# Performance work log

Hardware: AMD Instinct MI355X
Metric: run time of the kernel (lower is better)

## Reference

```python
import jax, jax.numpy as jnp
import numpy as np

TOP_K = 2


def setup_inputs() -> dict:
    key = jax.random.key(0)
    k1, k2, k3, k4 = jax.random.split(key, 4)
    B, S, D, H, E = 2, 2048, 1024, 4096, 8
    x = jax.random.normal(k1, (B, S, D), dtype=jnp.float32)
    router_w = jax.random.normal(k2, (E, D), dtype=jnp.float32) * 0.01  # nn.Linear(d, E).weight
    # kaiming-ish scaling for FFN weights
    w1 = jax.random.normal(k3, (E, H, D), dtype=jnp.float32) * (2.0 / D) ** 0.5
    b1 = jnp.zeros((E, H), dtype=jnp.float32)
    w2 = jax.random.normal(k4, (E, D, H), dtype=jnp.float32) * (2.0 / H) ** 0.5
    b2 = jnp.zeros((E, D), dtype=jnp.float32)
    return {"x": x, "router_w": router_w, "w1": w1, "b1": b1, "w2": w2, "b2": b2}


def reference(x, router_w, w1, b1, w2, b2):
    B, S, D = x.shape
    E = w1.shape[0]
    T = B * S
    x_flat = x.reshape(T, D)

    # Router: logits -> softmax -> top-k -> renormalize (eval mode: no jitter)
    logits = jnp.einsum('td,ed->te', x_flat, router_w)
    probs = jax.nn.softmax(logits, axis=-1)
    topw, topi = jax.lax.top_k(probs, TOP_K)                 # [T, k]
    topw = topw / jnp.sum(topw, axis=-1, keepdims=True)

    # Per-token combine weight for each expert: cw[t, e] = sum_k topw[t,k] * (topi[t,k]==e)
    cw = jnp.zeros((T, E), dtype=x.dtype)
    cw = cw.at[jnp.arange(T)[:, None], topi].add(topw)       # [T, E]

    # Expert FFNs (exact-erf GELU like torch F.gelu); combine weighted outputs.
    out = jnp.zeros((T, w2.shape[1]), dtype=x.dtype)
    for e in range(E):
        h = jax.nn.gelu(x_flat @ w1[e].T + b1[e], approximate=False)
        o = h @ w2[e].T + b2[e]
        out = out + cw[:, e:e + 1] * o
    return out.reshape(B, S, -1)
```

## Files before the change

kernel.cpp:

```cpp
#include <hip/hip_runtime.h>
#include <stdint.h>

typedef __attribute__((ext_vector_type(8))) short short8;
typedef __attribute__((ext_vector_type(4))) float floatx4;

#define T_TOK 4096
#define D_DIM 1024
#define H_DIM 4096
#define E_NUM 8
#define MAX_TILES 71

static __device__ __forceinline__ ushort f2bf(float f) {
    uint32_t u = __float_as_uint(f);
    u += 0x7FFF + ((u >> 16) & 1);
    return (ushort)(u >> 16);
}

static __device__ __forceinline__ uint4 pack8(float4 a, float4 b) {
    union { ushort u[8]; uint4 v; } r;
    r.u[0] = f2bf(a.x); r.u[1] = f2bf(a.y); r.u[2] = f2bf(a.z); r.u[3] = f2bf(a.w);
    r.u[4] = f2bf(b.x); r.u[5] = f2bf(b.y); r.u[6] = f2bf(b.z); r.u[7] = f2bf(b.w);
    return r.v;
}

static __device__ __forceinline__ void gl_lds16(const void* g, void* l) {
    __builtin_amdgcn_global_load_lds(
        (const __attribute__((address_space(1))) uint32_t*)g,
        (__attribute__((address_space(3))) uint32_t*)l, 16, 0, 0);
}

__global__ __launch_bounds__(256) void cvt_all_kernel(
    const float* __restrict__ x,  ushort* __restrict__ xbf,
    const float* __restrict__ w1, ushort* __restrict__ w1bf,
    const float* __restrict__ w2, ushort* __restrict__ w2bf)
{
    const size_t NX = (size_t)T_TOK * D_DIM;
    const size_t NW = (size_t)E_NUM * H_DIM * D_DIM;
    size_t i = ((size_t)blockIdx.x * 256 + threadIdx.x) * 8;
    const float* src; ushort* dst; size_t j;
    if (i < NX)           { src = x;  dst = xbf;  j = i; }
    else if (i < NX + NW) { src = w1; dst = w1bf; j = i - NX; }
    else                  { src = w2; dst = w2bf; j = i - NX - NW; }
    float4 a = *(const float4*)(src + j);
    float4 b = *(const float4*)(src + j + 4);
    *(uint4*)(dst + j) = pack8(a, b);
}

__global__ __launch_bounds__(256) void router_kernel(
    const float* __restrict__ x, const float* __restrict__ rw,
    int* __restrict__ counts, int* __restrict__ topi, float* __restrict__ topw)
{
    __shared__ float rwS[E_NUM * D_DIM];
    int tid = threadIdx.x;
    for (int i = tid; i < E_NUM * D_DIM / 4; i += 256)
        ((float4*)rwS)[i] = ((const float4*)rw)[i];
    __syncthreads();

    int wave = tid >> 6, lane = tid & 63;
    int t = blockIdx.x * 4 + wave;
    const float* xr = x + (size_t)t * D_DIM;

    float acc[E_NUM];
#pragma unroll
    for (int e = 0; e < E_NUM; e++) acc[e] = 0.f;

    float xv[16];
#pragma unroll
    for (int j = 0; j < 4; j++)
        *(float4*)&xv[j * 4] = ((const float4*)xr)[lane * 4 + j];
#pragma unroll
    for (int j = 0; j < 16; j++) {
        int idx = lane * 16 + j;
#pragma unroll
        for (int e = 0; e < E_NUM; e++)
            acc[e] += xv[j] * rwS[e * D_DIM + idx];
    }
#pragma unroll
    for (int e = 0; e < E_NUM; e++)
        for (int off = 32; off > 0; off >>= 1)
            acc[e] += __shfl_xor(acc[e], off, 64);

    if (lane == 0) {
        float mx = acc[0];
        for (int e = 1; e < E_NUM; e++) mx = fmaxf(mx, acc[e]);
        float p[E_NUM];
        for (int e = 0; e < E_NUM; e++) p[e] = expf(acc[e] - mx);
        int i0 = 0;
        for (int e = 1; e < E_NUM; e++) if (p[e] > p[i0]) i0 = e;
        int i1 = (i0 == 0) ? 1 : 0;
        for (int e = 0; e < E_NUM; e++) if (e != i0 && p[e] > p[i1]) i1 = e;
        float w0 = p[i0], w1 = p[i1], sw = w0 + w1;
        w0 /= sw; w1 /= sw;
        topi[t * 2] = i0; topi[t * 2 + 1] = i1;
        topw[t * 2] = w0; topw[t * 2 + 1] = w1;
        atomicAdd(&counts[i0], 1);
        atomicAdd(&counts[i1], 1);
    }
}

__global__ void offsets_tiles_kernel(const int* __restrict__ counts,
                                     int* __restrict__ offsets, int* __restrict__ cursors,
                                     int* __restrict__ tile_e, int* __restrict__ tile_m0)
{
    if (threadIdx.x == 0 && blockIdx.x == 0) {
        int off = 0, n = 0;
        for (int e = 0; e < E_NUM; e++) {
            offsets[e] = off; cursors[e] = off; off += counts[e];
            for (int m0 = 0; m0 < counts[e]; m0 += 128) {
                tile_e[n] = e; tile_m0[n] = m0; n++;
            }
        }
        for (; n < MAX_TILES; n++) tile_e[n] = -1;
    }
}

__global__ __launch_bounds__(256) void assign_kernel(
    const int* __restrict__ topi, const float* __restrict__ topw,
    int* __restrict__ cursors, int* __restrict__ pair_token, float* __restrict__ pair_w,
    int* __restrict__ ppos)
{
    int t = blockIdx.x * 256 + threadIdx.x;
    if (t >= T_TOK) return;
    for (int k = 0; k < 2; k++) {
        int e = topi[t * 2 + k];
        int pos = atomicAdd(&cursors[e], 1);
        pair_token[pos] = t;
        pair_w[pos] = topw[t * 2 + k];
        ppos[t * 2 + k] = pos;
    }
}

__global__ __launch_bounds__(256) void ffn1_kernel(
    const ushort* __restrict__ xbf, const ushort* __restrict__ w1bf,
    const float* __restrict__ bias1,
    const int* __restrict__ counts, const int* __restrict__ offsets,
    const int* __restrict__ tile_e, const int* __restrict__ tile_m0,
    const int* __restrict__ pair_token, ushort* __restrict__ h)
{
    int e = tile_e[blockIdx.x];
    if (e < 0) return;
    int m0 = tile_m0[blockIdx.x];
    int cnt = counts[e];
    int off = offsets[e];
    int n0 = blockIdx.y * 128;

    __shared__ ushort As[128 * 32];
    __shared__ ushort Bs[128 * 32];

    const int t = threadIdx.x;
    const int wave = t >> 6, lane = t & 63;
    const int wm = (wave >> 1) * 64, wn = (wave & 1) * 64;
    const int quad = lane >> 4, l16 = lane & 15;

    const int r0 = t >> 2;
    const int jb = t & 3;
    const int s0 = (r0 >> 1) & 3;
    const int csrc = (jb ^ s0) * 8;

    int grA0 = m0 + r0;        if (grA0 >= cnt) grA0 = cnt - 1;
    int grA1 = m0 + r0 + 64;   if (grA1 >= cnt) grA1 = cnt - 1;
    const ushort* aS0 = xbf + (size_t)pair_token[off + grA0] * D_DIM + csrc;
    const ushort* aS1 = xbf + (size_t)pair_token[off + grA1] * D_DIM + csrc;
    const ushort* bS0 = w1bf + ((size_t)e * H_DIM + n0 + r0) * D_DIM + csrc;
    const ushort* bS1 = bS0 + (size_t)64 * D_DIM;

    char* AsB = (char*)As;
    char* BsB = (char*)Bs;
    const int ldsW = wave * 1024;

    const int swz = (((l16 >> 1) & 3) ^ quad) * 16;
    int aOff[4], bOff[4];
#pragma unroll
    for (int i = 0; i < 4; i++) {
        aOff[i] = (wm + i * 16 + l16) * 64 + swz;
        bOff[i] = (wn + i * 16 + l16) * 64 + swz;
    }

    floatx4 acc[4][4] = {};

    for (int k0 = 0; k0 < D_DIM; k0 += 32) {
        __syncthreads();
        gl_lds16(aS0 + k0, AsB + ldsW);
        gl_lds16(aS1 + k0, AsB + 4096 + ldsW);
        gl_lds16(bS0 + k0, BsB + ldsW);
        gl_lds16(bS1 + k0, BsB + 4096 + ldsW);
        __syncthreads();

        short8 av[4], bv[4];
#pragma unroll
        for (int i = 0; i < 4; i++) av[i] = *(const short8*)(AsB + aOff[i]);
#pragma unroll
        for (int i = 0; i < 4; i++) bv[i] = *(const short8*)(BsB + bOff[i]);
#pragma unroll
        for (int mi = 0; mi < 4; mi++)
#pragma unroll
            for (int ni = 0; ni < 4; ni++)
                acc[mi][ni] = __builtin_amdgcn_mfma_f32_16x16x32_bf16(av[mi], bv[ni], acc[mi][ni], 0, 0, 0);
    }

    float bb[4];
#pragma unroll
    for (int ni = 0; ni < 4; ni++) bb[ni] = bias1[e * H_DIM + n0 + wn + ni * 16 + l16];

#pragma unroll
    for (int mi = 0; mi < 4; mi++) {
#pragma unroll
        for (int reg = 0; reg < 4; reg++) {
            int gm = m0 + wm + mi * 16 + quad * 4 + reg;
            if (gm < cnt) {
                ushort* hrow = h + (size_t)(off + gm) * H_DIM + n0 + wn;
#pragma unroll
                for (int ni = 0; ni < 4; ni++) {
                    float v = acc[mi][ni][reg] + bb[ni];
                    v = 0.5f * v * (1.f + erff(v * 0.70710678118654752f));
                    hrow[ni * 16 + l16] = f2bf(v);
                }
            }
        }
    }
}

__global__ __launch_bounds__(256) void ffn2_kernel(
    const ushort* __restrict__ h, const ushort* __restrict__ w2bf,
    const float* __restrict__ bias2,
    const int* __restrict__ counts, const int* __restrict__ offsets,
    const int* __restrict__ tile_e, const int* __restrict__ tile_m0,
    const float* __restrict__ pair_w, float* __restrict__ o_pair)
{
    int e = tile_e[blockIdx.x];
    if (e < 0) return;
    int m0 = tile_m0[blockIdx.x];
    int cnt = counts[e];
    int off = offsets[e];
    int n0 = blockIdx.y * 128;

    __shared__ ushort As[128 * 32];
    __shared__ ushort Bs[128 * 32];

    const int t = threadIdx.x;
    const int wave = t >> 6, lane = t & 63;
    const int wm = (wave >> 1) * 64, wn = (wave & 1) * 64;
    const int quad = lane >> 4, l16 = lane & 15;

    const int r0 = t >> 2;
    const int jb = t & 3;
    const int s0 = (r0 >> 1) & 3;
    const int csrc = (jb ^ s0) * 8;

    int grA0 = m0 + r0;        if (grA0 >= cnt) grA0 = cnt - 1;
    int grA1 = m0 + r0 + 64;   if (grA1 >= cnt) grA1 = cnt - 1;
    const ushort* aS0 = h + (size_t)(off + grA0) * H_DIM + csrc;
    const ushort* aS1 = h + (size_t)(off + grA1) * H_DIM + csrc;
    const ushort* bS0 = w2bf + ((size_t)e * D_DIM + n0 + r0) * H_DIM + csrc;
    const ushort* bS1 = bS0 + (size_t)64 * H_DIM;

    char* AsB = (char*)As;
    char* BsB = (char*)Bs;
    const int ldsW = wave * 1024;

    const int swz = (((l16 >> 1) & 3) ^ quad) * 16;
    int aOff[4], bOff[4];
#pragma unroll
    for (int i = 0; i < 4; i++) {
        aOff[i] = (wm + i * 16 + l16) * 64 + swz;
        bOff[i] = (wn + i * 16 + l16) * 64 + swz;
    }

    floatx4 acc[4][4] = {};

    for (int k0 = 0; k0 < H_DIM; k0 += 32) {
        __syncthreads();
        gl_lds16(aS0 + k0, AsB + ldsW);
        gl_lds16(aS1 + k0, AsB + 4096 + ldsW);
        gl_lds16(bS0 + k0, BsB + ldsW);
        gl_lds16(bS1 + k0, BsB + 4096 + ldsW);
        __syncthreads();

        short8 av[4], bv[4];
#pragma unroll
        for (int i = 0; i < 4; i++) av[i] = *(const short8*)(AsB + aOff[i]);
#pragma unroll
        for (int i = 0; i < 4; i++) bv[i] = *(const short8*)(BsB + bOff[i]);
#pragma unroll
        for (int mi = 0; mi < 4; mi++)
#pragma unroll
            for (int ni = 0; ni < 4; ni++)
                acc[mi][ni] = __builtin_amdgcn_mfma_f32_16x16x32_bf16(av[mi], bv[ni], acc[mi][ni], 0, 0, 0);
    }

    float bb[4];
#pragma unroll
    for (int ni = 0; ni < 4; ni++) bb[ni] = bias2[e * D_DIM + n0 + wn + ni * 16 + l16];

#pragma unroll
    for (int mi = 0; mi < 4; mi++) {
#pragma unroll
        for (int reg = 0; reg < 4; reg++) {
            int gm = m0 + wm + mi * 16 + quad * 4 + reg;
            if (gm < cnt) {
                float wgt = pair_w[off + gm];
                float* orow = o_pair + (size_t)(off + gm) * D_DIM + n0 + wn;
#pragma unroll
                for (int ni = 0; ni < 4; ni++)
                    orow[ni * 16 + l16] = (acc[mi][ni][reg] + bb[ni]) * wgt;
            }
        }
    }
}

__global__ __launch_bounds__(256) void combine_kernel(
    const float* __restrict__ o_pair, const int* __restrict__ ppos,
    float* __restrict__ out)
{
    int t = blockIdx.x;
    int d = threadIdx.x * 4;
    size_t p0 = (size_t)ppos[t * 2] * D_DIM;
    size_t p1 = (size_t)ppos[t * 2 + 1] * D_DIM;
    float4 a = *(const float4*)(o_pair + p0 + d);
    float4 b = *(const float4*)(o_pair + p1 + d);
    float4 r;
    r.x = a.x + b.x; r.y = a.y + b.y; r.z = a.z + b.z; r.w = a.w + b.w;
    *(float4*)(out + (size_t)t * D_DIM + d) = r;
}

extern "C" void kernel_launch(void* const* d_in, const int* in_sizes, int n_in,
                              void* d_out, int out_size, void* d_ws, size_t ws_size,
                              hipStream_t stream)
{
    const float* x  = (const float*)d_in[0];
    const float* rw = (const float*)d_in[1];
    const float* w1 = (const float*)d_in[2];
    const float* b1 = (const float*)d_in[3];
    const float* w2 = (const float*)d_in[4];
    const float* b2 = (const float*)d_in[5];
    float* out = (float*)d_out;

    char* ws = (char*)d_ws;
    int*   counts     = (int*)(ws + 0);
    int*   cursors    = (int*)(ws + 256);
    int*   offsets    = (int*)(ws + 512);
    int*   tile_e     = (int*)(ws + 1024);
    int*   tile_m0    = (int*)(ws + 1536);
    int*   topi       = (int*)(ws + 2048);
    float* topw       = (float*)(ws + 34816);
    int*   pair_token = (int*)(ws + 67584);
    float* pair_w     = (float*)(ws + 100352);
    int*   ppos       = (int*)(ws + 133120);
    ushort* xbf  = (ushort*)(ws + 165888);
    ushort* w1bf = (ushort*)(ws + 8554496ULL);
    ushort* w2bf = (ushort*)(ws + 75663360ULL);
    ushort* h    = (ushort*)(ws + 142772224ULL);
    float* o_pair = (float*)(ws + 8554496ULL);

    hipMemsetAsync(counts, 0, 32, stream);

    const size_t NTOT = (size_t)T_TOK * D_DIM + 2ULL * E_NUM * H_DIM * D_DIM;
    cvt_all_kernel<<<NTOT / 2048, 256, 0, stream>>>(x, xbf, w1, w1bf, w2, w2bf);

    router_kernel<<<T_TOK / 4, 256, 0, stream>>>(x, rw, counts, topi, topw);
    offsets_tiles_kernel<<<1, 64, 0, stream>>>(counts, offsets, cursors, tile_e, tile_m0);
    assign_kernel<<<T_TOK / 256, 256, 0, stream>>>(topi, topw, cursors, pair_token, pair_w, ppos);

    dim3 g1(MAX_TILES, H_DIM / 128, 1);
    ffn1_kernel<<<g1, 256, 0, stream>>>(xbf, w1bf, b1, counts, offsets, tile_e, tile_m0, pair_token, h);

    dim3 g2(MAX_TILES, D_DIM / 128, 1);
    ffn2_kernel<<<g2, 256, 0, stream>>>(h, w2bf, b2, counts, offsets, tile_e, tile_m0, pair_w, o_pair);

    combine_kernel<<<T_TOK, 256, 0, stream>>>(o_pair, ppos, out);
}
```

Before: 814.9 us.

## Double K-tile depth to 64 and split FFN2 K dimension across two planes

Both expert GEMM kernels now stage a 64-wide K slice per iteration with an 8-way XOR swizzle, halving barrier pairs per unit of work. FFN2 additionally splits its K=4096 reduction into two halves over gridDim.z and writes partial results to two separate planes, which the combine kernel sums. This raises FFN2 parallelism (its grid was only 71x8 tiles) at the cost of an extra fp32 partial-output write and read and doubled LDS usage per block.

```diff
diff --git a/kernel.cpp b/kernel.cpp
--- a/kernel.cpp
+++ b/kernel.cpp
@@ -9,6 +9,7 @@
 #define H_DIM 4096
 #define E_NUM 8
 #define MAX_TILES 71
+#define PLANE (8192ULL * 1024ULL)
 
 static __device__ __forceinline__ ushort f2bf(float f) {
     uint32_t u = __float_as_uint(f);
@@ -144,58 +145,67 @@
     int off = offsets[e];
     int n0 = blockIdx.y * 128;
 
-    __shared__ ushort As[128 * 32];
-    __shared__ ushort Bs[128 * 32];
+    __shared__ ushort As[128 * 64];
+    __shared__ ushort Bs[128 * 64];
 
     const int t = threadIdx.x;
     const int wave = t >> 6, lane = t & 63;
     const int wm = (wave >> 1) * 64, wn = (wave & 1) * 64;
     const int quad = lane >> 4, l16 = lane & 15;
 
-    const int r0 = t >> 2;
-    const int jb = t & 3;
-    const int s0 = (r0 >> 1) & 3;
-    const int csrc = (jb ^ s0) * 8;
-
-    int grA0 = m0 + r0;        if (grA0 >= cnt) grA0 = cnt - 1;
-    int grA1 = m0 + r0 + 64;   if (grA1 >= cnt) grA1 = cnt - 1;
-    const ushort* aS0 = xbf + (size_t)pair_token[off + grA0] * D_DIM + csrc;
-    const ushort* aS1 = xbf + (size_t)pair_token[off + grA1] * D_DIM + csrc;
-    const ushort* bS0 = w1bf + ((size_t)e * H_DIM + n0 + r0) * D_DIM + csrc;
-    const ushort* bS1 = bS0 + (size_t)64 * D_DIM;
-
+    const int rsub = lane >> 3;
+    const int cpos = lane & 7;
+    const int srcElem = (cpos ^ rsub) * 8;
+
+    const ushort* aP[4];
+    const ushort* bP[4];
+#pragma unroll
+    for (int j = 0; j < 4; j++) {
+        int row = j * 32 + wave * 8 + rsub;
+        int gr = m0 + row; if (gr >= cnt) gr = cnt - 1;
+        aP[j] = xbf + (size_t)pair_token[off + gr] * D_DIM + srcElem;
+        bP[j] = w1bf + ((size_t)e * H_DIM + n0 + row) * D_DIM + srcElem;
+    }
     char* AsB = (char*)As;
     char* BsB = (char*)Bs;
-    const int ldsW = wave * 1024;
-
-    const int swz = (((l16 >> 1) & 3) ^ quad) * 16;
-    int aOff[4], bOff[4];
+    int seg[4];
+#pragma unroll
+    for (int j = 0; j < 4; j++) seg[j] = j * 4096 + wave * 1024;
+
+    int rowA[4], rowB[4];
 #pragma unroll
     for (int i = 0; i < 4; i++) {
-        aOff[i] = (wm + i * 16 + l16) * 64 + swz;
-        bOff[i] = (wn + i * 16 + l16) * 64 + swz;
-    }
+        rowA[i] = (wm + i * 16 + l16) * 128;
+        rowB[i] = (wn + i * 16 + l16) * 128;
+    }
+    const int x7 = l16 & 7;
 
     floatx4 acc[4][4] = {};
 
-    for (int k0 = 0; k0 < D_DIM; k0 += 32) {
+    for (int k0 = 0; k0 < D_DIM; k0 += 64) {
         __syncthreads();
-        gl_lds16(aS0 + k0, AsB + ldsW);
-        gl_lds16(aS1 + k0, AsB + 4096 + ldsW);
-        gl_lds16(bS0 + k0, BsB + ldsW);
-        gl_lds16(bS1 + k0, BsB + 4096 + ldsW);
+#pragma unroll
+        for (int j = 0; j < 4; j++) gl_lds16(aP[j], AsB + seg[j]);
+#pragma unroll
+        for (int j = 0; j < 4; j++) gl_lds16(bP[j], BsB + seg[j]);
+#pragma unroll
+        for (int j = 0; j < 4; j++) { aP[j] += 64; bP[j] += 64; }
         __syncthreads();
 
-        short8 av[4], bv[4];
-#pragma unroll
-        for (int i = 0; i < 4; i++) av[i] = *(const short8*)(AsB + aOff[i]);
-#pragma unroll
-        for (int i = 0; i < 4; i++) bv[i] = *(const short8*)(BsB + bOff[i]);
-#pragma unroll
-        for (int mi = 0; mi < 4; mi++)
-#pragma unroll
-            for (int ni = 0; ni < 4; ni++)
-                acc[mi][ni] = __builtin_amdgcn_mfma_f32_16x16x32_bf16(av[mi], bv[ni], acc[mi][ni], 0, 0, 0);
+#pragma unroll
+        for (int kk = 0; kk < 2; kk++) {
+            const int co = ((((kk << 2) | quad)) ^ x7) << 4;
+            short8 av[4], bv[4];
+#pragma unroll
+            for (int i = 0; i < 4; i++) av[i] = *(const short8*)(AsB + rowA[i] + co);
+#pragma unroll
+            for (int i = 0; i < 4; i++) bv[i] = *(const short8*)(BsB + rowB[i] + co);
+#pragma unroll
+            for (int mi = 0; mi < 4; mi++)
+#pragma unroll
+                for (int ni = 0; ni < 4; ni++)
+                    acc[mi][ni] = __builtin_amdgcn_mfma_f32_16x16x32_bf16(av[mi], bv[ni], acc[mi][ni], 0, 0, 0);
+        }
     }
 
     float bb[4];
@@ -225,7 +235,7 @@
     const float* __restrict__ bias2,
     const int* __restrict__ counts, const int* __restrict__ offsets,
     const int* __restrict__ tile_e, const int* __restrict__ tile_m0,
-    const float* __restrict__ pair_w, float* __restrict__ o_pair)
+    const float* __restrict__ pair_w, float* __restrict__ o_part)
 {
     int e = tile_e[blockIdx.x];
     if (e < 0) return;
@@ -233,65 +243,78 @@
     int cnt = counts[e];
     int off = offsets[e];
     int n0 = blockIdx.y * 128;
-
-    __shared__ ushort As[128 * 32];
-    __shared__ ushort Bs[128 * 32];
+    int kc = blockIdx.z;
+    const size_t kbase = (size_t)kc * (H_DIM / 2);
+
+    __shared__ ushort As[128 * 64];
+    __shared__ ushort Bs[128 * 64];
 
     const int t = threadIdx.x;
     const int wave = t >> 6, lane = t & 63;
     const int wm = (wave >> 1) * 64, wn = (wave & 1) * 64;
     const int quad = lane >> 4, l16 = lane & 15;
 
-    const int r0 = t >> 2;
-    const int jb = t & 3;
-    const int s0 = (r0 >> 1) & 3;
-    const int csrc = (jb ^ s0) * 8;
-
-    int grA0 = m0 + r0;        if (grA0 >= cnt) grA0 = cnt - 1;
-    int grA1 = m0 + r0 + 64;   if (grA1 >= cnt) grA1 = cnt - 1;
-    const ushort* aS0 = h + (size_t)(off + grA0) * H_DIM + csrc;
-    const ushort* aS1 = h + (size_t)(off + grA1) * H_DIM + csrc;
-    const ushort* bS0 = w2bf + ((size_t)e * D_DIM + n0 + r0) * H_DIM + csrc;
-    const ushort* bS1 = bS0 + (size_t)64 * H_DIM;
-
+    const int rsub = lane >> 3;
+    const int cpos = lane & 7;
+    const int srcElem = (cpos ^ rsub) * 8;
+
+    const ushort* aP[4];
+    const ushort* bP[4];
+#pragma unroll
+    for (int j = 0; j < 4; j++) {
+        int row = j * 32 + wave * 8 + rsub;
+        int gr = m0 + row; if (gr >= cnt) gr = cnt - 1;
+        aP[j] = h + (size_t)(off + gr) * H_DIM + kbase + srcElem;
+        bP[j] = w2bf + ((size_t)e * D_DIM + n0 + row) * H_DIM + kbase + srcElem;
+    }
     char* AsB = (char*)As;
     char* BsB = (char*)Bs;
-    const int ldsW = wave * 1024;
-
-    const int swz = (((l16 >> 1) & 3) ^ quad) * 16;
-    int aOff[4], bOff[4];
+    int seg[4];
+#pragma unroll
+    for (int j = 0; j < 4; j++) seg[j] = j * 4096 + wave * 1024;
+
+    int rowA[4], rowB[4];
 #pragma unroll
     for (int i = 0; i < 4; i++) {
-        aOff[i] = (wm + i * 16 + l16) * 64 + swz;
-        bOff[i] = (wn + i * 16 + l16) * 64 + swz;
-    }
+        rowA[i] = (wm + i * 16 + l16) * 128;
+        rowB[i] = (wn + i * 16 + l16) * 128;
+    }
+    const int x7 = l16 & 7;
 
     floatx4 acc[4][4] = {};
 
-    for (int k0 = 0; k0 < H_DIM; k0 += 32) {
+    for (int k0 = 0; k0 < H_DIM / 2; k0 += 64) {
         __syncthreads();
-        gl_lds16(aS0 + k0, AsB + ldsW);
-        gl_lds16(aS1 + k0, AsB + 4096 + ldsW);
-        gl_lds16(bS0 + k0, BsB + ldsW);
-        gl_lds16(bS1 + k0, BsB + 4096 + ldsW);
+#pragma unroll
+        for (int j = 0; j < 4; j++) gl_lds16(aP[j], AsB + seg[j]);
+#pragma unroll
+        for (int j = 0; j < 4; j++) gl_lds16(bP[j], BsB + seg[j]);
+#pragma unroll
+        for (int j = 0; j < 4; j++) { aP[j] += 64; bP[j] += 64; }
         __syncthreads();
 
-        short8 av[4], bv[4];
-#pragma unroll
-        for (int i = 0; i < 4; i++) av[i] = *(const short8*)(AsB + aOff[i]);
-#pragma unroll
-        for (int i = 0; i < 4; i++) bv[i] = *(const short8*)(BsB + bOff[i]);
-#pragma unroll
-        for (int mi = 0; mi < 4; mi++)
-#pragma unroll
-            for (int ni = 0; ni < 4; ni++)
-                acc[mi][ni] = __builtin_amdgcn_mfma_f32_16x16x32_bf16(av[mi], bv[ni], acc[mi][ni], 0, 0, 0);
+#pragma unroll
+        for (int kk = 0; kk < 2; kk++) {
+            const int co = ((((kk << 2) | quad)) ^ x7) << 4;
+            short8 av[4], bv[4];
+#pragma unroll
+            for (int i = 0; i < 4; i++) av[i] = *(const short8*)(AsB + rowA[i] + co);
+#pragma unroll
+            for (int i = 0; i < 4; i++) bv[i] = *(const short8*)(BsB + rowB[i] + co);
+#pragma unroll
+            for (int mi = 0; mi < 4; mi++)
+#pragma unroll
+                for (int ni = 0; ni < 4; ni++)
+                    acc[mi][ni] = __builtin_amdgcn_mfma_f32_16x16x32_bf16(av[mi], bv[ni], acc[mi][ni], 0, 0, 0);
+        }
     }
 
     float bb[4];
 #pragma unroll
-    for (int ni = 0; ni < 4; ni++) bb[ni] = bias2[e * D_DIM + n0 + wn + ni * 16 + l16];
-
+    for (int ni = 0; ni < 4; ni++)
+        bb[ni] = (kc == 0) ? bias2[e * D_DIM + n0 + wn + ni * 16 + l16] : 0.f;
+
+    float* plane = o_part + (size_t)kc * PLANE;
 #pragma unroll
     for (int mi = 0; mi < 4; mi++) {
 #pragma unroll
@@ -299,7 +322,7 @@
             int gm = m0 + wm + mi * 16 + quad * 4 + reg;
             if (gm < cnt) {
                 float wgt = pair_w[off + gm];
-                float* orow = o_pair + (size_t)(off + gm) * D_DIM + n0 + wn;
+                float* orow = plane + (size_t)(off + gm) * D_DIM + n0 + wn;
 #pragma unroll
                 for (int ni = 0; ni < 4; ni++)
                     orow[ni * 16 + l16] = (acc[mi][ni][reg] + bb[ni]) * wgt;
@@ -309,17 +332,22 @@
 }
 
 __global__ __launch_bounds__(256) void combine_kernel(
-    const float* __restrict__ o_pair, const int* __restrict__ ppos,
+    const float* __restrict__ o_part, const int* __restrict__ ppos,
     float* __restrict__ out)
 {
     int t = blockIdx.x;
     int d = threadIdx.x * 4;
-    size_t p0 = (size_t)ppos[t * 2] * D_DIM;
-    size_t p1 = (size_t)ppos[t * 2 + 1] * D_DIM;
-    float4 a = *(const float4*)(o_pair + p0 + d);
-    float4 b = *(const float4*)(o_pair + p1 + d);
+    size_t p0 = (size_t)ppos[t * 2] * D_DIM + d;
+    size_t p1 = (size_t)ppos[t * 2 + 1] * D_DIM + d;
+    float4 a = *(const float4*)(o_part + p0);
+    float4 b = *(const float4*)(o_part + p1);
+    float4 c = *(const float4*)(o_part + PLANE + p0);
+    float4 e = *(const float4*)(o_part + PLANE + p1);
     float4 r;
-    r.x = a.x + b.x; r.y = a.y + b.y; r.z = a.z + b.z; r.w = a.w + b.w;
+    r.x = a.x + b.x + c.x + e.x;
+    r.y = a.y + b.y + c.y + e.y;
+    r.z = a.z + b.z + c.z + e.z;
+    r.w = a.w + b.w + c.w + e.w;
     *(float4*)(out + (size_t)t * D_DIM + d) = r;
 }
 
@@ -350,7 +378,7 @@
     ushort* w1bf = (ushort*)(ws + 8554496ULL);
     ushort* w2bf = (ushort*)(ws + 75663360ULL);
     ushort* h    = (ushort*)(ws + 142772224ULL);
-    float* o_pair = (float*)(ws + 8554496ULL);
+    float* o_part = (float*)(ws + 8554496ULL);
 
     hipMemsetAsync(counts, 0, 32, stream);
 
@@ -364,8 +392,8 @@
     dim3 g1(MAX_TILES, H_DIM / 128, 1);
     ffn1_kernel<<<g1, 256, 0, stream>>>(xbf, w1bf, b1, counts, offsets, tile_e, tile_m0, pair_token, h);
 
-    dim3 g2(MAX_TILES, D_DIM / 128, 1);
-    ffn2_kernel<<<g2, 256, 0, stream>>>(h, w2bf, b2, counts, offsets, tile_e, tile_m0, pair_w, o_pair);
-
-    combine_kernel<<<T_TOK, 256, 0, stream>>>(o_pair, ppos, out);
-}
+    dim3 g2(MAX_TILES, D_DIM / 128, 2);
+    ffn2_kernel<<<g2, 256, 0, stream>>>(h, w2bf, b2, counts, offsets, tile_e, tile_m0, pair_w, o_part);
+
+    combine_kernel<<<T_TOK, 256, 0, stream>>>(o_part, ppos, out);
+}
```

Result: no change. 819.7 us (+0.6%).
